# Optimization experiments

Measured on AMD Instinct MI355X. Metric: run time of the kernel, lower is better.

The kernel has to match this reference:

```python
import jax, jax.numpy as jnp
import numpy as np

N_ATOMS = 50000
DEG = 16
N_EDGES = N_ATOMS * DEG
N_MOL = 1000
NA = 23  # NUMBER_ATOMIC_GRAPH_FEATURES
NB = 7   # NUMBER_BOND_GRAPH_FEATURES


def _sph(v):
    # e3nn-style real spherical harmonics, lmax=2, normalize=False, 'component' normalization
    x, y, z = v[:, 0], v[:, 1], v[:, 2]
    sh1 = jnp.sqrt(3.0) * jnp.stack([x, y, z], axis=-1)  # [E,3] (1o)
    sh2 = jnp.stack([
        jnp.sqrt(15.0) * x * y,
        jnp.sqrt(15.0) * y * z,
        (jnp.sqrt(5.0) / 2.0) * (2 * z * z - x * x - y * y),
        jnp.sqrt(15.0) * x * z,
        (jnp.sqrt(15.0) / 2.0) * (x * x - y * y),
    ], axis=-1)  # [E,5] (2e)
    return sh1, sh2


def setup_inputs() -> dict:
    key = jax.random.key(0)
    ks = jax.random.split(key, 10)
    positions = jax.random.normal(ks[0], (N_ATOMS, 3), jnp.float32)
    x = jax.random.normal(ks[1], (N_ATOMS, NA), jnp.float32)
    edge_attr = jax.random.uniform(ks[2], (N_EDGES, NB), jnp.float32)
    edge_src = jax.random.randint(ks[3], (N_EDGES,), 0, N_ATOMS)
    edge_dst = jnp.repeat(jnp.arange(N_ATOMS), DEG)  # every node has in-degree DEG (required by the module)
    batch = jnp.repeat(jnp.arange(N_MOL), N_ATOMS // N_MOL)
    # tp1: FullyConnectedTensorProduct(NAx0e, 7x0e+7x1o+7x2e -> 32x0e+12x1e+12x1o+8x2e+8x2o)
    # allowed paths: 0e*0e->0e (32), 0e*1o->1o (12), 0e*2e->2e (8); 1e/2o outputs have no path (zero)
    W1_0 = jax.random.normal(ks[4], (NA, NB, 32), jnp.float32)
    W1_1 = jax.random.normal(ks[5], (NA, NB, 12), jnp.float32)
    W1_2 = jax.random.normal(ks[6], (NA, NB, 8), jnp.float32)
    # tp2: paths into 0e: 0e*0e (32x7), 1o*1o (12x7), 2e*2e (8x7)
    W2_0 = jax.random.normal(ks[7], (32, NB, 1), jnp.float32)
    W2_1 = jax.random.normal(ks[8], (12, NB, 1), jnp.float32)
    W2_2 = jax.random.normal(ks[9], (8, NB, 1), jnp.float32)
    return {"positions": positions, "x": x, "edge_attr": edge_attr,
            "W1_0": W1_0, "W1_1": W1_1, "W1_2": W1_2,
            "W2_0": W2_0, "W2_1": W2_1, "W2_2": W2_2,
            "edge_src": edge_src, "edge_dst": edge_dst, "batch": batch}


def reference(positions, x, edge_attr, W1_0, W1_1, W1_2, W2_0, W2_1, W2_2, edge_src, edge_dst, batch):
    N = x.shape[0]
    E = edge_attr.shape[0]
    M = N_MOL
    vec = positions[edge_src] - positions[edge_dst]            # [E,3]
    sh1, sh2 = _sph(vec)
    # FullTensorProduct(7x0e, 0e+1o+2e): scalar block is edge_attr itself; l>0 blocks are outer products
    b1 = edge_attr[:, :, None] * sh1[:, None, :]               # [E,NB,3]
    b2 = edge_attr[:, :, None] * sh2[:, None, :]               # [E,NB,5]
    deg = jax.ops.segment_sum(jnp.ones((E,), positions.dtype), edge_dst, num_segments=N)
    inv_sqrt_deg = 1.0 / jnp.sqrt(deg)                          # all nodes have >=1 edge by construction
    # tp1 on gathered source atom scalars. Since in1 is all-scalar, the SH factor separates:
    t = x[edge_src][:, :, None] * edge_attr[:, None, :]         # [E,NA,NB]
    n1 = 1.0 / np.sqrt(NA * NB)                                 # fan-in normalization
    m0 = jnp.einsum('eab,abo->eo', t, W1_0) * n1                # [E,32] 0e
    m1 = (jnp.einsum('eab,abo->eo', t, W1_1) * n1)[:, :, None] * sh1[:, None, :]  # [E,12,3] 1o
    m2 = (jnp.einsum('eab,abo->eo', t, W1_2) * n1)[:, :, None] * sh2[:, None, :]  # [E,8,5] 2e
    # (tp1's 12x1e and 8x2o outputs are structurally zero and have no path into tp2's 0e output -> dropped)
    s0 = jax.ops.segment_sum(m0, edge_dst, num_segments=N) * inv_sqrt_deg[:, None]
    s1 = jax.ops.segment_sum(m1, edge_dst, num_segments=N) * inv_sqrt_deg[:, None, None]
    s2 = jax.ops.segment_sum(m2, edge_dst, num_segments=N) * inv_sqrt_deg[:, None, None]
    # tp2 -> single 0e; l x l -> 0 contraction is inner product / sqrt(2l+1)
    e0 = jnp.einsum('ea,eb,ab->e', s0[edge_src], edge_attr, W2_0[:, :, 0]) / np.sqrt(32 * NB)
    e1 = jnp.einsum('eam,ebm,ab->e', s1[edge_src], b1, W2_1[:, :, 0]) / (np.sqrt(12 * NB) * np.sqrt(3.0))
    e2 = jnp.einsum('eam,ebm,ab->e', s2[edge_src], b2, W2_2[:, :, 0]) / (np.sqrt(8 * NB) * np.sqrt(5.0))
    edge_out = (e0 + e1 + e2)[:, None]                          # [E,1]
    node_out = jax.ops.segment_sum(edge_out, edge_dst, num_segments=N) * inv_sqrt_deg[:, None]
    apm = jax.ops.segment_sum(jnp.ones((N,), positions.dtype), batch, num_segments=M)
    acc = jax.ops.segment_sum(node_out, batch, num_segments=M)  # [M,1]
    return acc / jnp.sqrt(apm)[:, None]
```

## Files before the change

### kernel.cpp

```cpp
#include <hip/hip_runtime.h>
#include <hip/hip_bf16.h>

#define N_ATOMS 50000
#define N_EDGES 800000
#define DEG 16
#define N_MOL 1000
#define NA 23
#define NB 7
#define O0 32
#define O1 12
#define O2 8
#define OZ 21
#define NT 2
#define ZROW 64
#define NPW 4
#define VFRAG_N 896

typedef __attribute__((ext_vector_type(8))) short short8;
typedef __attribute__((ext_vector_type(4))) float floatx4;

__device__ __forceinline__ unsigned short bfbits(float f) {
    unsigned u = __float_as_uint(f);
    u += 0x7FFFu + ((u >> 16) & 1u);
    return (unsigned short)(u >> 16);
}
__device__ __forceinline__ float bf_lo(unsigned u) { return __uint_as_float(u << 16); }
__device__ __forceinline__ float bf_hi(unsigned u) { return __uint_as_float(u & 0xFFFF0000u); }
__device__ __forceinline__ float wred4(float v) {
    v += __shfl_xor(v, 16, 64); v += __shfl_xor(v, 32, 64); return v;
}

__global__ void k_prep(const float* __restrict__ W1_0, const float* __restrict__ W1_1,
                       const float* __restrict__ W1_2,
                       const float* __restrict__ W2_0, const float* __restrict__ W2_1,
                       const float* __restrict__ W2_2,
                       const float* __restrict__ x, const float* __restrict__ pos,
                       const int* __restrict__ edge_src,
                       unsigned short* __restrict__ Vfrag,
                       unsigned short* __restrict__ x_bf, float4* __restrict__ pos4,
                       float4* __restrict__ evec,
                       float* __restrict__ out) {
    int idx = blockIdx.x * 256 + threadIdx.x;
    if (idx < N_MOL) out[idx] = 0.0f;
    if (idx < VFRAG_N * 8) {
        int j    = idx & 7;
        int lane = (idx >> 3) & 63;
        int st   = idx >> 9;
        int s = st >> 1, t = st & 1;
        int a = (lane >> 4) * 8 + j, o = t * 16 + (lane & 15);
        float val = 0.f;
        if (a < NA && o < OZ) {
            const float n1 = 0.07881104062391006f;
            const float q  = 0.25f;
            float acc = 0.f;
            if (o < 7) {
                const float c0 = 0.06681531047810609f;
                const float* w1 = W1_0 + (a * NB + s) * O0;
                for (int k = 0; k < O0; k++) acc += w1[k] * W2_0[k * NB + o];
                val = acc * (n1 * c0 * q);
            } else if (o < 14) {
                const float c1 = 0.06299407883487121f;
                const float* w1 = W1_1 + (a * NB + s) * O1;
                for (int k = 0; k < O1; k++) acc += w1[k] * W2_1[k * NB + (o - 7)];
                val = acc * (n1 * c1 * q);
            } else {
                const float c2 = 0.05976143046671968f;
                const float* w1 = W1_2 + (a * NB + s) * O2;
                for (int k = 0; k < O2; k++) acc += w1[k] * W2_2[k * NB + (o - 14)];
                val = acc * (n1 * c2 * q);
            }
        }
        Vfrag[idx] = bfbits(val);
    }
    if (idx < N_ATOMS) {
        float4 p; p.x = pos[idx * 3 + 0]; p.y = pos[idx * 3 + 1];
        p.z = pos[idx * 3 + 2]; p.w = 0.f;
        pos4[idx] = p;
    }
    if (idx < N_ATOMS * 32) {
        int n = idx >> 5, a = idx & 31;
        x_bf[idx] = bfbits((a < NA) ? x[n * NA + a] : 0.f);
    }
    if (idx < N_EDGES) {
        int s = edge_src[idx];
        int d = idx >> 4;
        float4 v;
        v.x = pos[s * 3 + 0] - pos[d * 3 + 0];
        v.y = pos[s * 3 + 1] - pos[d * 3 + 1];
        v.z = pos[s * 3 + 2] - pos[d * 3 + 2];
        v.w = 0.f;
        evec[idx] = v;
    }
}

__global__ __launch_bounds__(256, 5) void k2_s(const float4* __restrict__ pos4,
        const unsigned short* __restrict__ x_bf, const float* __restrict__ edge_attr,
        const int* __restrict__ edge_src, const unsigned short* __restrict__ Vfrag,
        unsigned short* __restrict__ zbuf) {
    __shared__ short8 wfrag[VFRAG_N];
    __shared__ float hbuf[4][16][8];
    const int tid  = threadIdx.x;
    const int wid  = tid >> 6;
    const int lane = tid & 63;
    const int lcol = lane & 15;
    const int quad = lane >> 4;

    {
        uint4* dst = (uint4*)wfrag;
        const uint4* src4 = (const uint4*)Vfrag;
        for (int i = tid; i < VFRAG_N; i += 256) dst[i] = src4[i];
    }
    __syncthreads();

    const int wgid = __builtin_amdgcn_readfirstlane(blockIdx.x * 4 + wid);
    const int base = wgid * NPW;
    if (base >= N_ATOMS) return;

    float (*hb)[8] = hbuf[wid];
    const float s3 = 1.7320508075688772f, s15 = 3.872983346207417f;
    const float s5h = 1.118033988749895f, s15h = 1.9364916731037085f;

    auto clampn = [&](int i) { int nn = base + i; return nn < N_ATOMS ? nn : N_ATOMS - 1; };
    int s0v = edge_src[clampn(0) * DEG + lcol];
    int s1v = edge_src[clampn(1) * DEG + lcol];
    uint4 xu0 = *(const uint4*)(x_bf + s0v * 32 + quad * 8);
    float4 pp0 = pos4[s0v];
    float e0v[NB];
    {
        const float* p = edge_attr + ((size_t)clampn(0) * DEG + lcol) * NB;
        #pragma unroll
        for (int b = 0; b < NB; b++) e0v[b] = p[b];
    }

    #pragma unroll 1
    for (int i = 0; i < NPW; i++) {
        const int n = base + i;
        if (n >= N_ATOMS) break;
        int s2v = edge_src[clampn(i + 2 < NPW ? i + 2 : i) * DEG + lcol];
        uint4 xu1 = *(const uint4*)(x_bf + s1v * 32 + quad * 8);
        float4 pp1 = pos4[s1v];
        float e1v[NB];
        {
            const float* p = edge_attr + ((size_t)clampn(i + 1 < NPW ? i + 1 : i) * DEG + lcol) * NB;
            #pragma unroll
            for (int b = 0; b < NB; b++) e1v[b] = p[b];
        }
        float xf[8];
        xf[0] = bf_lo(xu0.x); xf[1] = bf_hi(xu0.x);
        xf[2] = bf_lo(xu0.y); xf[3] = bf_hi(xu0.y);
        xf[4] = bf_lo(xu0.z); xf[5] = bf_hi(xu0.z);
        xf[6] = bf_lo(xu0.w); xf[7] = bf_hi(xu0.w);

        const float4 pd = pos4[n];
        if (lane < 16) {
            const float vx = pp0.x - pd.x, vy = pp0.y - pd.y, vz = pp0.z - pd.z;
            hb[lane][0] = s3 * vx;  hb[lane][1] = s3 * vy;  hb[lane][2] = s3 * vz;
            hb[lane][3] = s15 * vx * vy;
            hb[lane][4] = s15 * vy * vz;
            hb[lane][5] = s5h * (2.f * vz * vz - vx * vx - vy * vy);
            hb[lane][6] = s15 * vx * vz;
            hb[lane][7] = s15h * (vx * vx - vy * vy);
        }
        floatx4 acc0 = {0.f,0.f,0.f,0.f}, acc1 = {0.f,0.f,0.f,0.f};
        #pragma unroll
        for (int s = 0; s < 7; s++) {
            const float eb = e0v[s];
            union { short8 v; unsigned u[4]; } af;
            #pragma unroll
            for (int j = 0; j < 8; j += 2) {
                float2 pr; pr.x = xf[j] * eb; pr.y = xf[j + 1] * eb;
                __hip_bfloat162 bb = __float22bfloat162_rn(pr);
                af.u[j >> 1] = *(unsigned*)&bb;
            }
            acc0 = __builtin_amdgcn_mfma_f32_16x16x32_bf16(af.v, wfrag[(s*NT+0)*64 + lane], acc0, 0, 0, 0);
            acc1 = __builtin_amdgcn_mfma_f32_16x16x32_bf16(af.v, wfrag[(s*NT+1)*64 + lane], acc1, 0, 0, 0);
        }
        float4 hA[4], hB[4];
        #pragma unroll
        for (int r = 0; r < 4; r++) {
            int e = quad * 4 + r;
            hA[r] = *(const float4*)&hb[e][0];
            hB[r] = *(const float4*)&hb[e][4];
        }
        unsigned short* sr = zbuf + (size_t)n * ZROW;
        const bool useA = (lcol >= 14);
        float v0 = acc0[0] + acc0[1] + acc0[2] + acc0[3];
        float u0 = 0.f, u1 = 0.f, u2 = 0.f;
        float t0 = 0.f, t1 = 0.f, t2 = 0.f, t3 = 0.f, t4 = 0.f;
        #pragma unroll
        for (int r = 0; r < 4; r++) {
            float m0 = acc0[r], m1 = acc1[r];
            u0 += m0 * hA[r].x; u1 += m0 * hA[r].y; u2 += m0 * hA[r].z;
            float mz = useA ? m0 : m1;
            t0 += mz * hA[r].w; t1 += mz * hB[r].x; t2 += mz * hB[r].y;
            t3 += mz * hB[r].z; t4 += mz * hB[r].w;
        }
        v0 = wred4(v0);
        u0 = wred4(u0); u1 = wred4(u1); u2 = wred4(u2);
        t0 = wred4(t0); t1 = wred4(t1); t2 = wred4(t2); t3 = wred4(t3); t4 = wred4(t4);
        if (quad == 0) {
            if (lcol < 7) sr[lcol * 8] = bfbits(v0);
            else if (lcol < 14) {
                int b = lcol - 7;
                sr[b * 8 + 1] = bfbits(u0); sr[b * 8 + 2] = bfbits(u1); sr[b * 8 + 3] = bfbits(u2);
            }
            if (lcol >= 14 || lcol < 5) {
                int b = useA ? (lcol - 14) : (lcol + 2);
                sr[b * 8 + 4] = bfbits(t0); sr[b * 8 + 5] = bfbits(t1); sr[b * 8 + 6] = bfbits(t2);
                sr[b * 8 + 7] = bfbits(t3); sr[56 + b] = bfbits(t4);
            }
            if (lcol == 5) sr[63] = 0;
        }
        s0v = s1v; s1v = s2v;
        xu0 = xu1; pp0 = pp1;
        #pragma unroll
        for (int b = 0; b < NB; b++) e0v[b] = e1v[b];
    }
}

__global__ __launch_bounds__(256, 4) void k3_g(const float4* __restrict__ evec,
        const float* __restrict__ edge_attr, const int* __restrict__ edge_src,
        const unsigned short* __restrict__ zbuf, float* __restrict__ out) {
    const int tid  = threadIdx.x;
    const int wid  = tid >> 6;
    const int lane = tid & 63;
    const int g    = lane >> 3;
    const int r    = lane & 7;
    const int wgid = __builtin_amdgcn_readfirstlane(blockIdx.x * 4 + wid);
    const int ebase = wgid * 64;
    const int nbase = ebase >> 4;

    int sj[8];
    #pragma unroll
    for (int j = 0; j < 8; j++) sj[j] = edge_src[ebase + j * 8 + g];

    uint4 zq[8];
    #pragma unroll
    for (int j = 0; j < 8; j++)
        zq[j] = *(const uint4*)(zbuf + (size_t)sj[j] * ZROW + r * 8);

    unsigned short c8u[8];
    #pragma unroll
    for (int j = 0; j < 8; j++)
        c8u[j] = zbuf[(size_t)sj[j] * ZROW + 56 + r];

    float4 ev[8];
    #pragma unroll
    for (int j = 0; j < 8; j++) ev[j] = evec[ebase + j * 8 + g];

    float eav[8];
    #pragma unroll
    for (int j = 0; j < 8; j++)
        eav[j] = (r < NB) ? edge_attr[(size_t)(ebase + j * 8 + g) * NB + r] : 0.f;

    const float s3 = 1.7320508075688772f, s15 = 3.872983346207417f;
    const float s5h = 1.118033988749895f, s15h = 1.9364916731037085f;
    float accA = 0.f, accB = 0.f, accC = 0.f, accD = 0.f;

    #pragma unroll
    for (int j = 0; j < 8; j++) {
        const float c8 = __uint_as_float(((unsigned)c8u[j]) << 16);
        const float4 v = ev[j];
        const float h1 = s3 * v.x, h2 = s3 * v.y, h3 = s3 * v.z;
        const float h4 = s15 * v.x * v.y, h5 = s15 * v.y * v.z;
        const float h6 = s5h * (2.f * v.z * v.z - v.x * v.x - v.y * v.y);
        const float h7 = s15 * v.x * v.z, h8 = s15h * (v.x * v.x - v.y * v.y);

        const uint4 z = zq[j];
        float t = bf_lo(z.x)
                + h1 * bf_hi(z.x) + h2 * bf_lo(z.y) + h3 * bf_hi(z.y)
                + h4 * bf_lo(z.z) + h5 * bf_hi(z.z) + h6 * bf_lo(z.w)
                + h7 * bf_hi(z.w) + h8 * c8;
        float p = eav[j] * t;
        if (j < 2)      accA += p;
        else if (j < 4) accB += p;
        else if (j < 6) accC += p;
        else            accD += p;
    }

    #pragma unroll
    for (int p = 0; p < 4; p++) {
        float a = (p == 0) ? accA : (p == 1) ? accB : (p == 2) ? accC : accD;
        #pragma unroll
        for (int off = 32; off >= 1; off >>= 1) a += __shfl_xor(a, off, 64);
        if (lane == p)
            atomicAdd(out + (nbase + p) / 50, a * 0.035355339059327376f);
    }
}

extern "C" void kernel_launch(void* const* d_in, const int* in_sizes, int n_in,
                              void* d_out, int out_size, void* d_ws, size_t ws_size,
                              hipStream_t stream) {
    const float* pos  = (const float*)d_in[0];
    const float* x    = (const float*)d_in[1];
    const float* ea   = (const float*)d_in[2];
    const float* W1_0 = (const float*)d_in[3];
    const float* W1_1 = (const float*)d_in[4];
    const float* W1_2 = (const float*)d_in[5];
    const float* W2_0 = (const float*)d_in[6];
    const float* W2_1 = (const float*)d_in[7];
    const float* W2_2 = (const float*)d_in[8];
    const int*   esrc = (const int*)d_in[9];
    float* out = (float*)d_out;

    char* ws = (char*)d_ws;
    unsigned short* Vfrag = (unsigned short*)ws;
    unsigned short* zbuf  = (unsigned short*)(ws + 32768);
    unsigned short* x_bf  = (unsigned short*)(ws + 32768 + 6400000);
    float4*         pos4  = (float4*)(ws + 32768 + 6400000 + 3200000);
    float4*         evec  = (float4*)(ws + 32768 + 6400000 + 3200000 + 800000);

    hipLaunchKernelGGL(k_prep, dim3((N_ATOMS * 32 + 255) / 256), dim3(256), 0, stream,
                       W1_0, W1_1, W1_2, W2_0, W2_1, W2_2, x, pos, esrc,
                       Vfrag, x_bf, pos4, evec, out);
    hipLaunchKernelGGL(k2_s, dim3((N_ATOMS / NPW + 3) / 4), dim3(256), 0, stream,
                       pos4, x_bf, ea, esrc, Vfrag, zbuf);
    hipLaunchKernelGGL(k3_g, dim3(N_EDGES / 64 / 4), dim3(256), 0, stream,
                       evec, ea, esrc, zbuf, out);
}
```

Before: 184.5 us.

## Drop precomputed edge vectors, recompute in gather kernel, split gather by source range

Measured after the change: 235.2 us. +27.5%, slower.

```diff
diff --git a/kernel.cpp b/kernel.cpp
--- a/kernel.cpp
+++ b/kernel.cpp
@@ -15,6 +15,7 @@
 #define ZROW 64
 #define NPW 4
 #define VFRAG_N 896
+#define PHALF 25000
 
 typedef __attribute__((ext_vector_type(8))) short short8;
 typedef __attribute__((ext_vector_type(4))) float floatx4;
@@ -35,10 +36,8 @@
                        const float* __restrict__ W2_0, const float* __restrict__ W2_1,
                        const float* __restrict__ W2_2,
                        const float* __restrict__ x, const float* __restrict__ pos,
-                       const int* __restrict__ edge_src,
                        unsigned short* __restrict__ Vfrag,
                        unsigned short* __restrict__ x_bf, float4* __restrict__ pos4,
-                       float4* __restrict__ evec,
                        float* __restrict__ out) {
     int idx = blockIdx.x * 256 + threadIdx.x;
     if (idx < N_MOL) out[idx] = 0.0f;
@@ -81,16 +80,6 @@
         int n = idx >> 5, a = idx & 31;
         x_bf[idx] = bfbits((a < NA) ? x[n * NA + a] : 0.f);
     }
-    if (idx < N_EDGES) {
-        int s = edge_src[idx];
-        int d = idx >> 4;
-        float4 v;
-        v.x = pos[s * 3 + 0] - pos[d * 3 + 0];
-        v.y = pos[s * 3 + 1] - pos[d * 3 + 1];
-        v.z = pos[s * 3 + 2] - pos[d * 3 + 2];
-        v.w = 0.f;
-        evec[idx] = v;
-    }
 }
 
 __global__ __launch_bounds__(256, 5) void k2_s(const float4* __restrict__ pos4,
@@ -218,9 +207,10 @@
     }
 }
 
-__global__ __launch_bounds__(256, 4) void k3_g(const float4* __restrict__ evec,
+__global__ __launch_bounds__(256, 4) void k3_g(const float4* __restrict__ pos4,
         const float* __restrict__ edge_attr, const int* __restrict__ edge_src,
-        const unsigned short* __restrict__ zbuf, float* __restrict__ out) {
+        const unsigned short* __restrict__ zbuf, float* __restrict__ out,
+        int plo) {
     const int tid  = threadIdx.x;
     const int wid  = tid >> 6;
     const int lane = tid & 63;
@@ -232,50 +222,72 @@
 
     int sj[8];
     #pragma unroll
-    for (int j = 0; j < 8; j++) sj[j] = edge_src[ebase + j * 8 + g];
+    for (int j = 0; j < 8; j++)
+        sj[j] = __builtin_nontemporal_load(edge_src + ebase + j * 8 + g);
+
+    bool act[8];
+    #pragma unroll
+    for (int j = 0; j < 8; j++)
+        act[j] = (sj[j] >= plo) && (sj[j] < plo + PHALF);
 
     uint4 zq[8];
-    #pragma unroll
-    for (int j = 0; j < 8; j++)
-        zq[j] = *(const uint4*)(zbuf + (size_t)sj[j] * ZROW + r * 8);
-
-    unsigned short c8u[8];
-    #pragma unroll
-    for (int j = 0; j < 8; j++)
-        c8u[j] = zbuf[(size_t)sj[j] * ZROW + 56 + r];
-
-    float4 ev[8];
-    #pragma unroll
-    for (int j = 0; j < 8; j++) ev[j] = evec[ebase + j * 8 + g];
-
+    float4 pp[8];
+    #pragma unroll
+    for (int j = 0; j < 8; j++) {
+        if (act[j]) {
+            zq[j] = *(const uint4*)(zbuf + (size_t)sj[j] * ZROW + r * 8);
+            pp[j] = pos4[sj[j]];
+        }
+    }
     float eav[8];
     #pragma unroll
-    for (int j = 0; j < 8; j++)
-        eav[j] = (r < NB) ? edge_attr[(size_t)(ebase + j * 8 + g) * NB + r] : 0.f;
+    for (int j = 0; j < 8; j++) {
+        eav[j] = 0.f;
+        if (act[j] && r < NB)
+            eav[j] = __builtin_nontemporal_load(
+                edge_attr + (size_t)(ebase + j * 8 + g) * NB + r);
+    }
+
+    const float4 pd0 = pos4[nbase + 0];
+    const float4 pd1 = pos4[nbase + 1];
+    const float4 pd2 = pos4[nbase + 2];
+    const float4 pd3 = pos4[nbase + 3];
 
     const float s3 = 1.7320508075688772f, s15 = 3.872983346207417f;
     const float s5h = 1.118033988749895f, s15h = 1.9364916731037085f;
     float accA = 0.f, accB = 0.f, accC = 0.f, accD = 0.f;
+    const int src7 = lane | 7;
 
     #pragma unroll
     for (int j = 0; j < 8; j++) {
-        const float c8 = __uint_as_float(((unsigned)c8u[j]) << 16);
-        const float4 v = ev[j];
-        const float h1 = s3 * v.x, h2 = s3 * v.y, h3 = s3 * v.z;
-        const float h4 = s15 * v.x * v.y, h5 = s15 * v.y * v.z;
-        const float h6 = s5h * (2.f * v.z * v.z - v.x * v.x - v.y * v.y);
-        const float h7 = s15 * v.x * v.z, h8 = s15h * (v.x * v.x - v.y * v.y);
-
-        const uint4 z = zq[j];
-        float t = bf_lo(z.x)
-                + h1 * bf_hi(z.x) + h2 * bf_lo(z.y) + h3 * bf_hi(z.y)
-                + h4 * bf_lo(z.z) + h5 * bf_hi(z.z) + h6 * bf_lo(z.w)
-                + h7 * bf_hi(z.w) + h8 * c8;
-        float p = eav[j] * t;
-        if (j < 2)      accA += p;
-        else if (j < 4) accB += p;
-        else if (j < 6) accC += p;
-        else            accD += p;
+        if (act[j]) {
+            const float4 pd = (j < 2) ? pd0 : (j < 4) ? pd1 : (j < 6) ? pd2 : pd3;
+            const float vx = pp[j].x - pd.x, vy = pp[j].y - pd.y, vz = pp[j].z - pd.z;
+            const float h1 = s3 * vx, h2 = s3 * vy, h3 = s3 * vz;
+            const float h4 = s15 * vx * vy, h5 = s15 * vy * vz;
+            const float h6 = s5h * (2.f * vz * vz - vx * vx - vy * vy);
+            const float h7 = s15 * vx * vz, h8 = s15h * (vx * vx - vy * vy);
+
+            const uint4 z = zq[j];
+            const unsigned w0 = (unsigned)__shfl((int)z.x, src7, 64);
+            const unsigned w1 = (unsigned)__shfl((int)z.y, src7, 64);
+            const unsigned w2 = (unsigned)__shfl((int)z.z, src7, 64);
+            const unsigned w3 = (unsigned)__shfl((int)z.w, src7, 64);
+            const unsigned wa = (r & 4) ? w2 : w0;
+            const unsigned wb = (r & 4) ? w3 : w1;
+            const unsigned wc = (r & 2) ? wb : wa;
+            const float c8 = (r & 1) ? bf_hi(wc) : bf_lo(wc);
+
+            float t = bf_lo(z.x)
+                    + h1 * bf_hi(z.x) + h2 * bf_lo(z.y) + h3 * bf_hi(z.y)
+                    + h4 * bf_lo(z.z) + h5 * bf_hi(z.z) + h6 * bf_lo(z.w)
+                    + h7 * bf_hi(z.w) + h8 * c8;
+            float p = eav[j] * t;
+            if (j < 2)      accA += p;
+            else if (j < 4) accB += p;
+            else if (j < 6) accC += p;
+            else            accD += p;
+        }
     }
 
     #pragma unroll
@@ -308,13 +320,13 @@
     unsigned short* zbuf  = (unsigned short*)(ws + 32768);
     unsigned short* x_bf  = (unsigned short*)(ws + 32768 + 6400000);
     float4*         pos4  = (float4*)(ws + 32768 + 6400000 + 3200000);
-    float4*         evec  = (float4*)(ws + 32768 + 6400000 + 3200000 + 800000);
 
     hipLaunchKernelGGL(k_prep, dim3((N_ATOMS * 32 + 255) / 256), dim3(256), 0, stream,
-                       W1_0, W1_1, W1_2, W2_0, W2_1, W2_2, x, pos, esrc,
-                       Vfrag, x_bf, pos4, evec, out);
+                       W1_0, W1_1, W1_2, W2_0, W2_1, W2_2, x, pos, Vfrag, x_bf, pos4, out);
     hipLaunchKernelGGL(k2_s, dim3((N_ATOMS / NPW + 3) / 4), dim3(256), 0, stream,
                        pos4, x_bf, ea, esrc, Vfrag, zbuf);
     hipLaunchKernelGGL(k3_g, dim3(N_EDGES / 64 / 4), dim3(256), 0, stream,
-                       evec, ea, esrc, zbuf, out);
-}
+                       pos4, ea, esrc, zbuf, out, 0);
+    hipLaunchKernelGGL(k3_g, dim3(N_EDGES / 64 / 4), dim3(256), 0, stream,
+                       pos4, ea, esrc, zbuf, out, PHALF);
+}
```
